# Performance work log

Hardware: AMD Instinct MI355X
Metric: run time of the kernel (lower is better)

Reference implementation:

```python
import jax, jax.numpy as jnp
import numpy as np

N = 50000
D_IN = 128
HID = 128
HEADS = 4
PER_HEAD = HID // HEADS
NEG_SLOPE = 0.2


def gatv2_conv(x, src, dst, W_l, W_r, att, bias, H, C, n):
    """PyG GATv2Conv: x [n,F], src/dst [E] (self-loops already appended).
    out[i] = sum_{j->i} softmax_i(att . leaky_relu(Wl x_j + Wr x_i)) * (Wl x_j)
    """
    x_l = (x @ W_l).reshape(n, H, C)  # source-side transform
    x_r = (x @ W_r).reshape(n, H, C)  # destination-side transform
    e = jax.nn.leaky_relu(x_l[src] + x_r[dst], NEG_SLOPE)      # [E,H,C]
    alpha = jnp.einsum('ehc,hc->eh', e, att)                    # [E,H]
    # segment softmax over incoming edges of each destination node
    seg_max = jax.ops.segment_max(alpha, dst, num_segments=n)   # [n,H]
    alpha = jnp.exp(alpha - seg_max[dst])
    denom = jax.ops.segment_sum(alpha, dst, num_segments=n)     # [n,H]
    alpha = alpha / denom[dst]
    msg = x_l[src] * alpha[..., None]                           # [E,H,C]
    out = jax.ops.segment_sum(msg, dst, num_segments=n)         # [n,H,C]
    return out.reshape(n, H * C) + bias


def setup_inputs() -> dict:
    key = jax.random.key(0)
    ks = jax.random.split(key, 10)
    E = 800000
    x = jax.random.normal(ks[0], (N, D_IN), dtype=jnp.float32)
    edge_index = jax.random.randint(ks[1], (2, E), 0, N, dtype=jnp.int64)

    def glorot(k, shape):
        lim = float(np.sqrt(6.0 / (shape[0] + shape[1])))
        return jax.random.uniform(k, shape, jnp.float32, -lim, lim)

    # layer 1: GATv2Conv(D_IN, PER_HEAD, heads=HEADS, concat=True)
    W_l1 = glorot(ks[2], (D_IN, HEADS * PER_HEAD))
    W_r1 = glorot(ks[3], (D_IN, HEADS * PER_HEAD))
    att1 = glorot(ks[4], (HEADS, PER_HEAD))
    b1 = jnp.zeros((HEADS * PER_HEAD,), jnp.float32)
    # layer 2: GATv2Conv(HID, HID, heads=1, concat=True)
    W_l2 = glorot(ks[5], (HID, HID))
    W_r2 = glorot(ks[6], (HID, HID))
    att2 = glorot(ks[7], (1, HID))
    b2 = jnp.zeros((HID,), jnp.float32)
    return {"x": x, "edge_index": edge_index,
            "W_l1": W_l1, "W_r1": W_r1, "att1": att1, "b1": b1,
            "W_l2": W_l2, "W_r2": W_r2, "att2": att2, "b2": b2}


def reference(x, edge_index, W_l1, W_r1, att1, b1, W_l2, W_r2, att2, b2):
    # add self-loops (PyG GATv2Conv default add_self_loops=True)
    loops = jnp.arange(N, dtype=edge_index.dtype)
    src = jnp.concatenate([edge_index[0], loops])
    dst = jnp.concatenate([edge_index[1], loops])
    h = gatv2_conv(x, src, dst, W_l1, W_r1, att1, b1, HEADS, PER_HEAD, N)
    h = jax.nn.relu(h)
    out = gatv2_conv(h, src, dst, W_l2, W_r2, att2, b2, 1, HID, N)
    return out
```

## Files before the change

### kernel.cpp

```cpp
#include <hip/hip_runtime.h>
#include <hip/hip_fp16.h>
#include <math.h>


#define NEG_SLOPE 0.2f
#define CHUNKS 128
#define DCAP 8192

typedef _Float16 half8 __attribute__((ext_vector_type(8)));
typedef _Float16 half2v __attribute__((ext_vector_type(2)));
typedef float floatx4 __attribute__((ext_vector_type(4)));

#if defined(__has_builtin)
#if __has_builtin(__builtin_amdgcn_fdot2)
#define HAVE_FDOT2 1
#endif
#endif

template <int CTRL>
__device__ __forceinline__ float dppmov(float x) {
    int xi = __builtin_bit_cast(int, x);
    int r  = __builtin_amdgcn_update_dpp(0, xi, CTRL, 0xF, 0xF, true);
    return __builtin_bit_cast(float, r);
}
#define DPP_XOR1  0xB1
#define DPP_XOR2  0x4E
#define DPP_HMIRR 0x141
#define DPP_MIRR  0x140


__global__ __launch_bounds__(256)
void sortA_hist(const int* __restrict__ dstA, int* __restrict__ hist_mat,
                int E, int Et, int csz) {
    __shared__ int hist[256];
    int tid = threadIdx.x, c = blockIdx.x;
    hist[tid] = 0;
    __syncthreads();
    int start = c * csz, stop = min(Et, start + csz);
    for (int e = start + tid; e < stop; e += 256) {
        int d = (e < E) ? dstA[e] : (e - E);
        atomicAdd(&hist[d >> 8], 1);
    }
    __syncthreads();
    hist_mat[c * 256 + tid] = hist[tid];
}

__global__ __launch_bounds__(1024)
void sortB_scan(const int* __restrict__ hist_mat, int* __restrict__ offs_flat) {
    __shared__ int wsum[16];
    int t = threadIdx.x;
    int lane = t & 63, wid = t >> 6;
    int carry = 0;
    for (int it = 0; it < 8; ++it) {
        int f0 = it * 4096 + t * 4;
        int v[4];
        #pragma unroll
        for (int k = 0; k < 4; ++k) {
            int f = f0 + k;
            v[k] = hist_mat[(f & 127) * 256 + (f >> 7)];
        }
        int s1 = v[0] + v[1], s2 = s1 + v[2], s3 = s2 + v[3];
        int x = s3;
        #pragma unroll
        for (int off = 1; off < 64; off <<= 1) {
            int y = __shfl_up(x, off, 64);
            if (lane >= off) x += y;
        }
        if (lane == 63) wsum[wid] = x;
        __syncthreads();
        if (wid == 0) {
            int s = (lane < 16) ? wsum[lane] : 0;
            #pragma unroll
            for (int off = 1; off < 16; off <<= 1) {
                int y = __shfl_up(s, off, 64);
                if (lane >= off) s += y;
            }
            if (lane < 16) wsum[lane] = s;
        }
        __syncthreads();
        int woff = (wid == 0) ? 0 : wsum[wid - 1];
        int excl = carry + woff + x - s3;
        offs_flat[f0 + 0] = excl;
        offs_flat[f0 + 1] = excl + v[0];
        offs_flat[f0 + 2] = excl + s1;
        offs_flat[f0 + 3] = excl + s2;
        carry += wsum[15];
        __syncthreads();
    }
}

__global__ __launch_bounds__(256)
void sortC_scatter(const int* __restrict__ srcA, const int* __restrict__ dstA,
                   const int* __restrict__ offs_flat, int* __restrict__ packed,
                   int E, int Et, int csz) {
    __shared__ int pos[256];
    int tid = threadIdx.x, c = blockIdx.x;
    pos[tid] = offs_flat[tid * CHUNKS + c];
    __syncthreads();
    int start = c * csz, stop = min(Et, start + csz);
    for (int e = start + tid; e < stop; e += 256) {
        int s, d;
        if (e < E) { s = srcA[e]; d = dstA[e]; } else { s = e - E; d = s; }
        int p = atomicAdd(&pos[d >> 8], 1);
        packed[p] = ((d & 255) << 16) | s;
    }
}

__global__ __launch_bounds__(256)
void sortD_fine(const int* __restrict__ offs_flat, const int* __restrict__ packed,
                int* __restrict__ rowptr, int* __restrict__ srcs,
                int n, int Et, int nbuck) {
    __shared__ int stage[DCAP];
    __shared__ int sorted[DCAP];
    __shared__ int hist[256], curv[256], wsumD[4];
    int tid = threadIdx.x, b = blockIdx.x;
    int base = offs_flat[b * CHUNKS];
    int end  = (b == nbuck - 1) ? Et : offs_flat[(b + 1) * CHUNKS];
    int m = min(end - base, DCAP);

    hist[tid] = 0;
    for (int i = tid; i < m; i += 256) stage[i] = packed[base + i];
    __syncthreads();
    for (int i = tid; i < m; i += 256) atomicAdd(&hist[stage[i] >> 16], 1);
    __syncthreads();
    {
        int v = hist[tid];
        int lane = tid & 63, w = tid >> 6;
        int x = v;
        #pragma unroll
        for (int off = 1; off < 64; off <<= 1) {
            int y = __shfl_up(x, off, 64);
            if (lane >= off) x += y;
        }
        if (lane == 63) wsumD[w] = x;
        __syncthreads();
        int woff = 0;
        for (int i = 0; i < w; ++i) woff += wsumD[i];
        int excl = woff + x - v;
        curv[tid] = excl;
        int node0 = b << 8;
        if (node0 + tid < n) rowptr[node0 + tid] = base + excl;
        if (b == 0 && tid == 0) rowptr[n] = Et;
    }
    __syncthreads();
    for (int i = tid; i < m; i += 256) {
        int p = stage[i];
        int pos = atomicAdd(&curv[p >> 16], 1);
        sorted[pos] = p & 0xFFFF;
    }
    __syncthreads();
    for (int i = tid; i < m; i += 256) srcs[base + i] = sorted[i];
}


__global__ __launch_bounds__(256)
void convert_w2(const float* __restrict__ Wl1, const float* __restrict__ Wr1,
                const float* __restrict__ Wl2, const float* __restrict__ Wr2,
                const float* __restrict__ att1, const float* __restrict__ att2,
                _Float16* __restrict__ Wt1, _Float16* __restrict__ Wt2,
                _Float16* __restrict__ attH) {
    int t = blockIdx.x * blockDim.x + threadIdx.x;
    if (t < 65536) {
        int layer = t >> 15;
        int id = t & 32767;
        int c = id >> 7, k = id & 127;
        const float* Wl = layer ? Wl2 : Wl1;
        const float* Wr = layer ? Wr2 : Wr1;
        _Float16* Wt = layer ? Wt2 : Wt1;
        float v = (c < 128) ? Wl[(size_t)k * 128 + c] : Wr[(size_t)k * 128 + (c - 128)];
        Wt[(size_t)c * 128 + k] = (_Float16)v;
    } else {
        int id = t - 65536;
        if (id < 256) {
            float v = (id < 128) ? att1[id] : att2[id - 128];
            attH[id] = (_Float16)v;
        }
    }
}

#define BPAD 136

template <bool AF32>
__global__ __launch_bounds__(256)
void gemm_mfma(const void* __restrict__ Av, const _Float16* __restrict__ Bt,
               _Float16* __restrict__ outL, _Float16* __restrict__ outR, int n) {
    __shared__ _Float16 sB[256 * BPAD];
    int tid = threadIdx.x;
    {
        int c0 = (tid & 15) * 8;
        int r0 = tid >> 4;
        #pragma unroll
        for (int i = 0; i < 16; ++i) {
            int r = r0 + i * 16;
            *(half8*)(sB + r * BPAD + c0) = *(const half8*)(Bt + (size_t)r * 128 + c0);
        }
    }
    int wave = tid >> 6;
    int lane = tid & 63;
    int ln = lane & 15;
    int q  = lane >> 4;
    int row0 = blockIdx.x * 64 + wave * 16;

    int arow = row0 + ln;
    if (arow >= n) arow = n - 1;
    half8 a0, a1, a2, a3;
    if (AF32) {
        const float* ap = (const float*)Av + (size_t)arow * 128 + q * 8;
        #pragma unroll
        for (int g = 0; g < 4; ++g) {
            float4 f0 = *(const float4*)(ap + g * 32);
            float4 f1 = *(const float4*)(ap + g * 32 + 4);
            half8 h;
            h[0] = (_Float16)f0.x; h[1] = (_Float16)f0.y;
            h[2] = (_Float16)f0.z; h[3] = (_Float16)f0.w;
            h[4] = (_Float16)f1.x; h[5] = (_Float16)f1.y;
            h[6] = (_Float16)f1.z; h[7] = (_Float16)f1.w;
            if (g == 0) a0 = h; else if (g == 1) a1 = h;
            else if (g == 2) a2 = h; else a3 = h;
        }
    } else {
        const _Float16* ap = (const _Float16*)Av + (size_t)arow * 128 + q * 8;
        a0 = *(const half8*)(ap);
        a1 = *(const half8*)(ap + 32);
        a2 = *(const half8*)(ap + 64);
        a3 = *(const half8*)(ap + 96);
    }

    __syncthreads();

    floatx4 acc[16];
    #pragma unroll
    for (int ct = 0; ct < 16; ++ct) {
        const _Float16* bp = sB + (ct * 16 + ln) * BPAD + q * 8;
        half8 b0 = *(const half8*)(bp);
        half8 b1 = *(const half8*)(bp + 32);
        half8 b2 = *(const half8*)(bp + 64);
        half8 b3 = *(const half8*)(bp + 96);
        floatx4 c = {0.f, 0.f, 0.f, 0.f};
        c = __builtin_amdgcn_mfma_f32_16x16x32_f16(a0, b0, c, 0, 0, 0);
        c = __builtin_amdgcn_mfma_f32_16x16x32_f16(a1, b1, c, 0, 0, 0);
        c = __builtin_amdgcn_mfma_f32_16x16x32_f16(a2, b2, c, 0, 0, 0);
        c = __builtin_amdgcn_mfma_f32_16x16x32_f16(a3, b3, c, 0, 0, 0);
        acc[ct] = c;
    }

    #pragma unroll
    for (int ct = 0; ct < 16; ++ct) {
        int col = ct * 16 + ln;
        #pragma unroll
        for (int r = 0; r < 4; ++r) {
            int grow = row0 + q * 4 + r;
            if (grow < n) {
                _Float16 v = (_Float16)acc[ct][r];
                if (ct < 8) outL[(size_t)grow * 128 + col] = v;
                else        outR[(size_t)grow * 128 + (col - 128)] = v;
            }
        }
    }
}


template <bool LAYER1>
__global__ __launch_bounds__(256)
void edge_aggregate(const _Float16* __restrict__ xl, const _Float16* __restrict__ xr,
                    const _Float16* __restrict__ attH, const float* __restrict__ bias,
                    const int* __restrict__ rowptr, const int* __restrict__ srcs,
                    void* __restrict__ outv, int n) {
    int node = blockIdx.x * (blockDim.x >> 6) + (threadIdx.x >> 6);
    int lane = threadIdx.x & 63;
    if (node >= n) return;
    int ln = lane & 15;
    int q  = lane >> 4;
    int c0 = ln * 8;

    half8 xrh = *(const half8*)(xr + (size_t)node * 128 + c0);
    half8 ahh = *(const half8*)(attH + c0);

    float acc[8] = {0.f, 0.f, 0.f, 0.f, 0.f, 0.f, 0.f, 0.f};
    float l = 0.f;

    auto proc = [&](half8 vh, bool valid) {
        half8 e  = vh + xrh;
        half8 es = e * (_Float16)NEG_SLOPE;
        half8 lr = __builtin_elementwise_max(e, es);
        float p = 0.f;
        #pragma unroll
        for (int k = 0; k < 4; ++k) {
            half2v ee = { lr[2 * k], lr[2 * k + 1] };
            half2v aa = { ahh[2 * k], ahh[2 * k + 1] };
#ifdef HAVE_FDOT2
            p = __builtin_amdgcn_fdot2(ee, aa, p, false);
#else
            p = fmaf((float)ee[0], (float)aa[0], p);
            p = fmaf((float)ee[1], (float)aa[1], p);
#endif
        }
        p += dppmov<DPP_XOR1>(p);
        p += dppmov<DPP_XOR2>(p);
        if (!LAYER1) { p += dppmov<DPP_HMIRR>(p); p += dppmov<DPP_MIRR>(p); }
        float pe = __expf(p);
        if (!valid) pe = 0.f;
        l += pe;
        #pragma unroll
        for (int k = 0; k < 8; ++k) acc[k] = fmaf(pe, (float)vh[k], acc[k]);
    };

    int jb = rowptr[node], je = rowptr[node + 1];
    for (int base = jb; base < je; base += 64) {
        int idx = base + lane;
        int myS = (idx < je) ? srcs[idx] : 0;
        int cnt = min(64, je - base);
        int t = 0;
        for (; t + 8 <= cnt; t += 8) {
            int sa = __shfl(myS, t + q, 64);
            int sb = __shfl(myS, t + 4 + q, 64);
            half8 va = *(const half8*)(xl + (size_t)sa * 128 + c0);
            half8 vb = *(const half8*)(xl + (size_t)sb * 128 + c0);
            proc(va, true);
            proc(vb, true);
        }
        for (; t < cnt; t += 4) {
            int sa = __shfl(myS, t + q, 64);
            half8 va = *(const half8*)(xl + (size_t)sa * 128 + c0);
            proc(va, (t + q) < cnt);
        }
    }

    #pragma unroll
    for (int k = 0; k < 8; ++k) {
        acc[k] += __shfl_xor(acc[k], 16, 64);
        acc[k] += __shfl_xor(acc[k], 32, 64);
    }
    l += __shfl_xor(l, 16, 64);
    l += __shfl_xor(l, 32, 64);

    float inv = 1.0f / l;
    float bv[8];
    *(float4*)&bv[0] = *(const float4*)(bias + c0);
    *(float4*)&bv[4] = *(const float4*)(bias + c0 + 4);
    float o[8];
    #pragma unroll
    for (int k = 0; k < 8; ++k) {
        o[k] = acc[k] * inv + bv[k];
        if (LAYER1) o[k] = fmaxf(o[k], 0.f);
    }
    if (lane < 16) {
        if (LAYER1) {
            __half2 hh2[4];
            #pragma unroll
            for (int k = 0; k < 4; ++k) hh2[k] = __floats2half2_rn(o[2 * k], o[2 * k + 1]);
            *(float4*)((_Float16*)outv + (size_t)node * 128 + c0) = *(float4*)&hh2[0];
        } else {
            float* out = (float*)outv;
            *(float4*)(out + (size_t)node * 128 + c0)     = *(float4*)&o[0];
            *(float4*)(out + (size_t)node * 128 + c0 + 4) = *(float4*)&o[4];
        }
    }
}


extern "C" void kernel_launch(void* const* d_in, const int* in_sizes, int n_in,
                              void* d_out, int out_size, void* d_ws, size_t ws_size,
                              hipStream_t stream) {
    const float* x    = (const float*)d_in[0];
    const int*   ei   = (const int*)d_in[1];
    const float* Wl1  = (const float*)d_in[2];
    const float* Wr1  = (const float*)d_in[3];
    const float* att1 = (const float*)d_in[4];
    const float* b1   = (const float*)d_in[5];
    const float* Wl2  = (const float*)d_in[6];
    const float* Wr2  = (const float*)d_in[7];
    const float* att2 = (const float*)d_in[8];
    const float* b2   = (const float*)d_in[9];

    int n  = in_sizes[0] / 128;
    int E  = in_sizes[1] / 2;
    int Et = E + n;

    _Float16* xlh  = (_Float16*)d_ws;
    _Float16* xrh2 = xlh + (size_t)n * 128;
    _Float16* hh   = xrh2 + (size_t)n * 128;
    _Float16* Wt1  = hh  + (size_t)n * 128;
    _Float16* Wt2  = Wt1 + 256 * 128;
    _Float16* attH = Wt2 + 256 * 128;
    int* rowptr   = (int*)(attH + 256);
    int* srcs     = rowptr + (n + 1);
    int* packed   = srcs + Et;
    int* hist_mat = packed + Et;
    int* offs_flat= hist_mat + CHUNKS * 256;

    const int* srcA = ei;
    const int* dstA = ei + E;

    int csz   = (Et + CHUNKS - 1) / CHUNKS;
    int nbuck = (n + 255) >> 8;

    sortA_hist<<<CHUNKS, 256, 0, stream>>>(dstA, hist_mat, E, Et, csz);
    sortB_scan<<<1, 1024, 0, stream>>>(hist_mat, offs_flat);
    sortC_scatter<<<CHUNKS, 256, 0, stream>>>(srcA, dstA, offs_flat, packed, E, Et, csz);
    sortD_fine<<<nbuck, 256, 0, stream>>>(offs_flat, packed, rowptr, srcs, n, Et, nbuck);

    convert_w2<<<257, 256, 0, stream>>>(Wl1, Wr1, Wl2, Wr2, att1, att2, Wt1, Wt2, attH);

    int gemm_grid = (n + 63) / 64;
    int edge_grid = (n + 3) / 4;

    gemm_mfma<true><<<gemm_grid, 256, 0, stream>>>(x, Wt1, xlh, xrh2, n);
    edge_aggregate<true><<<edge_grid, 256, 0, stream>>>(
        xlh, xrh2, attH, b1, rowptr, srcs, hh, n);

    gemm_mfma<false><<<gemm_grid, 256, 0, stream>>>(hh, Wt2, xlh, xrh2, n);
    edge_aggregate<false><<<edge_grid, 256, 0, stream>>>(
        xlh, xrh2, attH + 128, b2, rowptr, srcs, d_out, n);
}
```

Baseline: 238.1 us.

## Merge independent sort, weight-convert and GEMM stages into shared launches; unroll gather

The weight conversion now runs in the same launch as the coarse histogram, and the layer-1 GEMM runs in the same launch as the scatter pass. Both are done with block-index dispatch, which cuts the number of kernel launches and lets independent work overlap on the GPU. The edge-aggregate gather loop now processes 16 edges per iteration instead of 8, putting more loads in flight. The fused kernels take the larger shared-memory footprint of the two bodies, which may reduce occupancy for the sort blocks.

```diff
diff --git a/kernel.cpp b/kernel.cpp
--- a/kernel.cpp
+++ b/kernel.cpp
@@ -29,11 +29,11 @@
 #define DPP_MIRR  0x140
 
 
-__global__ __launch_bounds__(256)
-void sortA_hist(const int* __restrict__ dstA, int* __restrict__ hist_mat,
-                int E, int Et, int csz) {
+__device__ __forceinline__ void sortA_body(int c, const int* __restrict__ dstA,
+                                           int* __restrict__ hist_mat,
+                                           int E, int Et, int csz) {
     __shared__ int hist[256];
-    int tid = threadIdx.x, c = blockIdx.x;
+    int tid = threadIdx.x;
     hist[tid] = 0;
     __syncthreads();
     int start = c * csz, stop = min(Et, start + csz);
@@ -45,121 +45,12 @@
     hist_mat[c * 256 + tid] = hist[tid];
 }
 
-__global__ __launch_bounds__(1024)
-void sortB_scan(const int* __restrict__ hist_mat, int* __restrict__ offs_flat) {
-    __shared__ int wsum[16];
-    int t = threadIdx.x;
-    int lane = t & 63, wid = t >> 6;
-    int carry = 0;
-    for (int it = 0; it < 8; ++it) {
-        int f0 = it * 4096 + t * 4;
-        int v[4];
-        #pragma unroll
-        for (int k = 0; k < 4; ++k) {
-            int f = f0 + k;
-            v[k] = hist_mat[(f & 127) * 256 + (f >> 7)];
-        }
-        int s1 = v[0] + v[1], s2 = s1 + v[2], s3 = s2 + v[3];
-        int x = s3;
-        #pragma unroll
-        for (int off = 1; off < 64; off <<= 1) {
-            int y = __shfl_up(x, off, 64);
-            if (lane >= off) x += y;
-        }
-        if (lane == 63) wsum[wid] = x;
-        __syncthreads();
-        if (wid == 0) {
-            int s = (lane < 16) ? wsum[lane] : 0;
-            #pragma unroll
-            for (int off = 1; off < 16; off <<= 1) {
-                int y = __shfl_up(s, off, 64);
-                if (lane >= off) s += y;
-            }
-            if (lane < 16) wsum[lane] = s;
-        }
-        __syncthreads();
-        int woff = (wid == 0) ? 0 : wsum[wid - 1];
-        int excl = carry + woff + x - s3;
-        offs_flat[f0 + 0] = excl;
-        offs_flat[f0 + 1] = excl + v[0];
-        offs_flat[f0 + 2] = excl + s1;
-        offs_flat[f0 + 3] = excl + s2;
-        carry += wsum[15];
-        __syncthreads();
-    }
-}
-
-__global__ __launch_bounds__(256)
-void sortC_scatter(const int* __restrict__ srcA, const int* __restrict__ dstA,
-                   const int* __restrict__ offs_flat, int* __restrict__ packed,
-                   int E, int Et, int csz) {
-    __shared__ int pos[256];
-    int tid = threadIdx.x, c = blockIdx.x;
-    pos[tid] = offs_flat[tid * CHUNKS + c];
-    __syncthreads();
-    int start = c * csz, stop = min(Et, start + csz);
-    for (int e = start + tid; e < stop; e += 256) {
-        int s, d;
-        if (e < E) { s = srcA[e]; d = dstA[e]; } else { s = e - E; d = s; }
-        int p = atomicAdd(&pos[d >> 8], 1);
-        packed[p] = ((d & 255) << 16) | s;
-    }
-}
-
-__global__ __launch_bounds__(256)
-void sortD_fine(const int* __restrict__ offs_flat, const int* __restrict__ packed,
-                int* __restrict__ rowptr, int* __restrict__ srcs,
-                int n, int Et, int nbuck) {
-    __shared__ int stage[DCAP];
-    __shared__ int sorted[DCAP];
-    __shared__ int hist[256], curv[256], wsumD[4];
-    int tid = threadIdx.x, b = blockIdx.x;
-    int base = offs_flat[b * CHUNKS];
-    int end  = (b == nbuck - 1) ? Et : offs_flat[(b + 1) * CHUNKS];
-    int m = min(end - base, DCAP);
-
-    hist[tid] = 0;
-    for (int i = tid; i < m; i += 256) stage[i] = packed[base + i];
-    __syncthreads();
-    for (int i = tid; i < m; i += 256) atomicAdd(&hist[stage[i] >> 16], 1);
-    __syncthreads();
-    {
-        int v = hist[tid];
-        int lane = tid & 63, w = tid >> 6;
-        int x = v;
-        #pragma unroll
-        for (int off = 1; off < 64; off <<= 1) {
-            int y = __shfl_up(x, off, 64);
-            if (lane >= off) x += y;
-        }
-        if (lane == 63) wsumD[w] = x;
-        __syncthreads();
-        int woff = 0;
-        for (int i = 0; i < w; ++i) woff += wsumD[i];
-        int excl = woff + x - v;
-        curv[tid] = excl;
-        int node0 = b << 8;
-        if (node0 + tid < n) rowptr[node0 + tid] = base + excl;
-        if (b == 0 && tid == 0) rowptr[n] = Et;
-    }
-    __syncthreads();
-    for (int i = tid; i < m; i += 256) {
-        int p = stage[i];
-        int pos = atomicAdd(&curv[p >> 16], 1);
-        sorted[pos] = p & 0xFFFF;
-    }
-    __syncthreads();
-    for (int i = tid; i < m; i += 256) srcs[base + i] = sorted[i];
-}
-
-
-__global__ __launch_bounds__(256)
-void convert_w2(const float* __restrict__ Wl1, const float* __restrict__ Wr1,
-                const float* __restrict__ Wl2, const float* __restrict__ Wr2,
-                const float* __restrict__ att1, const float* __restrict__ att2,
-                _Float16* __restrict__ Wt1, _Float16* __restrict__ Wt2,
-                _Float16* __restrict__ attH) {
-    int t = blockIdx.x * blockDim.x + threadIdx.x;
+__device__ __forceinline__ void convert_body(int t,
+        const float* __restrict__ Wl1, const float* __restrict__ Wr1,
+        const float* __restrict__ Wl2, const float* __restrict__ Wr2,
+        const float* __restrict__ att1, const float* __restrict__ att2,
+        _Float16* __restrict__ Wt1, _Float16* __restrict__ Wt2,
+        _Float16* __restrict__ attH) {
     if (t < 65536) {
         int layer = t >> 15;
         int id = t & 32767;
@@ -178,12 +69,28 @@
     }
 }
 
+__device__ __forceinline__ void sortC_body(int c, const int* __restrict__ srcA,
+        const int* __restrict__ dstA, const int* __restrict__ offs_flat,
+        int* __restrict__ packed, int E, int Et, int csz) {
+    __shared__ int pos[256];
+    int tid = threadIdx.x;
+    pos[tid] = offs_flat[tid * CHUNKS + c];
+    __syncthreads();
+    int start = c * csz, stop = min(Et, start + csz);
+    for (int e = start + tid; e < stop; e += 256) {
+        int s, d;
+        if (e < E) { s = srcA[e]; d = dstA[e]; } else { s = e - E; d = s; }
+        int p = atomicAdd(&pos[d >> 8], 1);
+        packed[p] = ((d & 255) << 16) | s;
+    }
+}
+
 #define BPAD 136
 
 template <bool AF32>
-__global__ __launch_bounds__(256)
-void gemm_mfma(const void* __restrict__ Av, const _Float16* __restrict__ Bt,
-               _Float16* __restrict__ outL, _Float16* __restrict__ outR, int n) {
+__device__ __forceinline__ void gemm_body(int bid, const void* __restrict__ Av,
+        const _Float16* __restrict__ Bt, _Float16* __restrict__ outL,
+        _Float16* __restrict__ outR, int n) {
     __shared__ _Float16 sB[256 * BPAD];
     int tid = threadIdx.x;
     {
@@ -199,7 +106,7 @@
     int lane = tid & 63;
     int ln = lane & 15;
     int q  = lane >> 4;
-    int row0 = blockIdx.x * 64 + wave * 16;
+    int row0 = bid * 64 + wave * 16;
 
     int arow = row0 + ln;
     if (arow >= n) arow = n - 1;
@@ -260,6 +167,132 @@
 }
 
 
+__global__ __launch_bounds__(256)
+void fused_pre(const int* __restrict__ dstA, int* __restrict__ hist_mat,
+               int E, int Et, int csz,
+               const float* __restrict__ Wl1, const float* __restrict__ Wr1,
+               const float* __restrict__ Wl2, const float* __restrict__ Wr2,
+               const float* __restrict__ att1, const float* __restrict__ att2,
+               _Float16* __restrict__ Wt1, _Float16* __restrict__ Wt2,
+               _Float16* __restrict__ attH) {
+    if (blockIdx.x < CHUNKS) {
+        sortA_body(blockIdx.x, dstA, hist_mat, E, Et, csz);
+    } else {
+        int t = (blockIdx.x - CHUNKS) * 256 + threadIdx.x;
+        convert_body(t, Wl1, Wr1, Wl2, Wr2, att1, att2, Wt1, Wt2, attH);
+    }
+}
+
+__global__ __launch_bounds__(1024)
+void sortB_scan(const int* __restrict__ hist_mat, int* __restrict__ offs_flat) {
+    __shared__ int wsum[16];
+    int t = threadIdx.x;
+    int lane = t & 63, wid = t >> 6;
+    int carry = 0;
+    for (int it = 0; it < 8; ++it) {
+        int f0 = it * 4096 + t * 4;
+        int v[4];
+        #pragma unroll
+        for (int k = 0; k < 4; ++k) {
+            int f = f0 + k;
+            v[k] = hist_mat[(f & 127) * 256 + (f >> 7)];
+        }
+        int s1 = v[0] + v[1], s2 = s1 + v[2], s3 = s2 + v[3];
+        int x = s3;
+        #pragma unroll
+        for (int off = 1; off < 64; off <<= 1) {
+            int y = __shfl_up(x, off, 64);
+            if (lane >= off) x += y;
+        }
+        if (lane == 63) wsum[wid] = x;
+        __syncthreads();
+        if (wid == 0) {
+            int s = (lane < 16) ? wsum[lane] : 0;
+            #pragma unroll
+            for (int off = 1; off < 16; off <<= 1) {
+                int y = __shfl_up(s, off, 64);
+                if (lane >= off) s += y;
+            }
+            if (lane < 16) wsum[lane] = s;
+        }
+        __syncthreads();
+        int woff = (wid == 0) ? 0 : wsum[wid - 1];
+        int excl = carry + woff + x - s3;
+        offs_flat[f0 + 0] = excl;
+        offs_flat[f0 + 1] = excl + v[0];
+        offs_flat[f0 + 2] = excl + s1;
+        offs_flat[f0 + 3] = excl + s2;
+        carry += wsum[15];
+        __syncthreads();
+    }
+}
+
+__global__ __launch_bounds__(256)
+void fused_mid(const int* __restrict__ srcA, const int* __restrict__ dstA,
+               const int* __restrict__ offs_flat, int* __restrict__ packed,
+               int E, int Et, int csz,
+               const float* __restrict__ X, const _Float16* __restrict__ Wt1,
+               _Float16* __restrict__ outL, _Float16* __restrict__ outR, int n) {
+    if (blockIdx.x < CHUNKS) {
+        sortC_body(blockIdx.x, srcA, dstA, offs_flat, packed, E, Et, csz);
+    } else {
+        gemm_body<true>(blockIdx.x - CHUNKS, X, Wt1, outL, outR, n);
+    }
+}
+
+__global__ __launch_bounds__(256)
+void gemm_l2(const _Float16* __restrict__ A, const _Float16* __restrict__ Bt,
+             _Float16* __restrict__ outL, _Float16* __restrict__ outR, int n) {
+    gemm_body<false>(blockIdx.x, A, Bt, outL, outR, n);
+}
+
+__global__ __launch_bounds__(256)
+void sortD_fine(const int* __restrict__ offs_flat, const int* __restrict__ packed,
+                int* __restrict__ rowptr, int* __restrict__ srcs,
+                int n, int Et, int nbuck) {
+    __shared__ int stage[DCAP];
+    __shared__ int sorted[DCAP];
+    __shared__ int hist[256], curv[256], wsumD[4];
+    int tid = threadIdx.x, b = blockIdx.x;
+    int base = offs_flat[b * CHUNKS];
+    int end  = (b == nbuck - 1) ? Et : offs_flat[(b + 1) * CHUNKS];
+    int m = min(end - base, DCAP);
+
+    hist[tid] = 0;
+    for (int i = tid; i < m; i += 256) stage[i] = packed[base + i];
+    __syncthreads();
+    for (int i = tid; i < m; i += 256) atomicAdd(&hist[stage[i] >> 16], 1);
+    __syncthreads();
+    {
+        int v = hist[tid];
+        int lane = tid & 63, w = tid >> 6;
+        int x = v;
+        #pragma unroll
+        for (int off = 1; off < 64; off <<= 1) {
+            int y = __shfl_up(x, off, 64);
+            if (lane >= off) x += y;
+        }
+        if (lane == 63) wsumD[w] = x;
+        __syncthreads();
+        int woff = 0;
+        for (int i = 0; i < w; ++i) woff += wsumD[i];
+        int excl = woff + x - v;
+        curv[tid] = excl;
+        int node0 = b << 8;
+        if (node0 + tid < n) rowptr[node0 + tid] = base + excl;
+        if (b == 0 && tid == 0) rowptr[n] = Et;
+    }
+    __syncthreads();
+    for (int i = tid; i < m; i += 256) {
+        int p = stage[i];
+        int pos = atomicAdd(&curv[p >> 16], 1);
+        sorted[pos] = p & 0xFFFF;
+    }
+    __syncthreads();
+    for (int i = tid; i < m; i += 256) srcs[base + i] = sorted[i];
+}
+
+
 template <bool LAYER1>
 __global__ __launch_bounds__(256)
 void edge_aggregate(const _Float16* __restrict__ xl, const _Float16* __restrict__ xr,
@@ -311,13 +344,16 @@
         int myS = (idx < je) ? srcs[idx] : 0;
         int cnt = min(64, je - base);
         int t = 0;
-        for (; t + 8 <= cnt; t += 8) {
-            int sa = __shfl(myS, t + q, 64);
-            int sb = __shfl(myS, t + 4 + q, 64);
-            half8 va = *(const half8*)(xl + (size_t)sa * 128 + c0);
-            half8 vb = *(const half8*)(xl + (size_t)sb * 128 + c0);
-            proc(va, true);
-            proc(vb, true);
+        for (; t + 16 <= cnt; t += 16) {
+            int s0 = __shfl(myS, t + q, 64);
+            int s1 = __shfl(myS, t + 4 + q, 64);
+            int s2 = __shfl(myS, t + 8 + q, 64);
+            int s3 = __shfl(myS, t + 12 + q, 64);
+            half8 v0 = *(const half8*)(xl + (size_t)s0 * 128 + c0);
+            half8 v1 = *(const half8*)(xl + (size_t)s1 * 128 + c0);
+            half8 v2 = *(const half8*)(xl + (size_t)s2 * 128 + c0);
+            half8 v3 = *(const half8*)(xl + (size_t)s3 * 128 + c0);
+            proc(v0, true); proc(v1, true); proc(v2, true); proc(v3, true);
         }
         for (; t < cnt; t += 4) {
             int sa = __shfl(myS, t + q, 64);
@@ -394,22 +430,20 @@
 
     int csz   = (Et + CHUNKS - 1) / CHUNKS;
     int nbuck = (n + 255) >> 8;
-
-    sortA_hist<<<CHUNKS, 256, 0, stream>>>(dstA, hist_mat, E, Et, csz);
-    sortB_scan<<<1, 1024, 0, stream>>>(hist_mat, offs_flat);
-    sortC_scatter<<<CHUNKS, 256, 0, stream>>>(srcA, dstA, offs_flat, packed, E, Et, csz);
-    sortD_fine<<<nbuck, 256, 0, stream>>>(offs_flat, packed, rowptr, srcs, n, Et, nbuck);
-
-    convert_w2<<<257, 256, 0, stream>>>(Wl1, Wr1, Wl2, Wr2, att1, att2, Wt1, Wt2, attH);
-
     int gemm_grid = (n + 63) / 64;
     int edge_grid = (n + 3) / 4;
 
-    gemm_mfma<true><<<gemm_grid, 256, 0, stream>>>(x, Wt1, xlh, xrh2, n);
+    fused_pre<<<CHUNKS + 257, 256, 0, stream>>>(
+        dstA, hist_mat, E, Et, csz,
+        Wl1, Wr1, Wl2, Wr2, att1, att2, Wt1, Wt2, attH);
+    sortB_scan<<<1, 1024, 0, stream>>>(hist_mat, offs_flat);
+    fused_mid<<<CHUNKS + gemm_grid, 256, 0, stream>>>(
+        srcA, dstA, offs_flat, packed, E, Et, csz,
+        x, Wt1, xlh, xrh2, n);
+    sortD_fine<<<nbuck, 256, 0, stream>>>(offs_flat, packed, rowptr, srcs, n, Et, nbuck);
     edge_aggregate<true><<<edge_grid, 256, 0, stream>>>(
         xlh, xrh2, attH, b1, rowptr, srcs, hh, n);
-
-    gemm_mfma<false><<<gemm_grid, 256, 0, stream>>>(hh, Wt2, xlh, xrh2, n);
+    gemm_l2<<<gemm_grid, 256, 0, stream>>>(hh, Wt2, xlh, xrh2, n);
     edge_aggregate<false><<<edge_grid, 256, 0, stream>>>(
         xlh, xrh2, attH + 128, b2, rowptr, srcs, d_out, n);
 }
```

Measured after the change: 223.9 us. -6.0%, faster.
